# Kernel tuning notes

Measured on AMD Instinct MI355X. Metric: run time of the kernel, lower is better.

## Reference

```python
import jax, jax.numpy as jnp
import numpy as np

KNOTS = 17  # integration points on [0, 3]


def _buffers():
    t = jnp.linspace(0.0, 3.0, KNOTS, dtype=jnp.float32)
    dt = 3.0 / (KNOTS - 1)
    w = jnp.full((KNOTS,), 2.0 * dt, dtype=jnp.float32)
    w = w.at[0].set(dt).at[-1].set(dt)          # trapezoid-style end weights
    phi = jnp.exp(-jnp.square(t) / 2.0)         # ideal Gaussian ECF
    return t, phi, w * phi


def setup_inputs() -> dict:
    key = jax.random.key(0)
    k1, k2 = jax.random.split(key)
    N, D, P = 8192, 512, 1024
    z = jax.random.normal(k1, (N, D), dtype=jnp.float32)
    A = jax.random.normal(k2, (D, P), dtype=jnp.float32)  # random projections (hoisted from forward)
    return {"z": z, "A": A}


def reference(z, A):
    t, phi, weights = _buffers()
    D = z.shape[-1]
    flat = z.reshape(-1, D).astype(jnp.float32)            # [N, D]
    An = A / jnp.clip(jnp.linalg.norm(A, axis=0, keepdims=True), 1e-8)
    proj = flat @ An                                       # [N, P]
    x_t = proj[:, :, None] * t                             # [N, P, K]
    cos_mean = jnp.mean(jnp.cos(x_t), axis=0)              # [P, K]
    sin_mean = jnp.mean(jnp.sin(x_t), axis=0)              # [P, K]
    err = jnp.square(cos_mean - phi) + jnp.square(sin_mean)
    statistic = (err @ weights) * flat.shape[0]            # [P]
    return jnp.mean(statistic)
```

## Files before the change

kernel.cpp:

```cpp
#include <hip/hip_runtime.h>
#include <stdint.h>

#define N_SAMP 8192
#define D_DIM  512
#define P_DIM  1024
#define DT     0.1875f

typedef float f32x4 __attribute__((ext_vector_type(4)));
typedef float f32x2 __attribute__((ext_vector_type(2)));
typedef short bf16x8 __attribute__((ext_vector_type(8)));
typedef unsigned short u16;

__device__ __forceinline__ u16 f2bf(float x){
    unsigned int u = __float_as_uint(x);
    return (u16)((u + 0x7FFFu + ((u >> 16) & 1u)) >> 16);
}

__device__ __forceinline__ void load_lds16(const void* g, void* l){
    __builtin_amdgcn_global_load_lds(
        (const __attribute__((address_space(1))) void*)(uintptr_t)g,
        (__attribute__((address_space(3))) void*)(uint32_t)(uintptr_t)l,
        16, 0, 0);
}

__global__ __launch_bounds__(256) void k_prep(const float4* __restrict__ z4,
                                              u16* __restrict__ zb,
                                              const float* __restrict__ A,
                                              float* __restrict__ inv,
                                              u16* __restrict__ AnT,
                                              float* __restrict__ gpart,
                                              float* __restrict__ out){
    const int tid = threadIdx.x;
    const int b = blockIdx.x;
    if (b < 4096){
        int i = b * 256 + tid;
        if (i == 0) out[0] = 0.f;
        float4 v = z4[i];
        ushort4 o;
        o.x = f2bf(v.x); o.y = f2bf(v.y); o.z = f2bf(v.z); o.w = f2bf(v.w);
        ((ushort4*)zb)[i] = o;
        return;
    }
    if (b < 4128){
        __shared__ float red[8][32];
        const int p0 = (b - 4096) * 32;
        const int pl = tid & 31, dg = tid >> 5;
        float s = 0.f;
        #pragma unroll 8
        for (int i = 0; i < 64; ++i){
            float v = A[(size_t)(dg + 8 * i) * P_DIM + p0 + pl];
            s += v * v;
        }
        red[dg][pl] = s;
        __syncthreads();
        if (tid < 32){
            float t = 0.f;
            #pragma unroll
            for (int g = 0; g < 8; ++g) t += red[g][tid];
            inv[p0 + tid] = 1.0f / fmaxf(sqrtf(t), 1e-8f);
        }
        return;
    }
    if (b < 4640){
        __shared__ float tile[32][33];
        const int t = b - 4128;
        const int p0 = (t & 31) * 32, d0 = (t >> 5) * 32;
        const int tx = tid & 31, ty = tid >> 5;
        #pragma unroll
        for (int j = 0; j < 4; ++j)
            tile[ty + j * 8][tx] = A[(size_t)(d0 + ty + j * 8) * P_DIM + p0 + tx];
        __syncthreads();
        #pragma unroll
        for (int j = 0; j < 4; ++j){
            int pp = ty + j * 8;
            AnT[(size_t)(p0 + pp) * D_DIM + d0 + tx] = f2bf(tile[tx][pp]);
        }
        return;
    }
    int i = (b - 4640) * 256 + tid;
    ((float4*)gpart)[i] = (float4){0.f, 0.f, 0.f, 0.f};
}

__global__ __launch_bounds__(512) void k_gemm_ecf(const u16* __restrict__ zb,
                                                  const u16* __restrict__ AnT,
                                                  const float* __restrict__ inv,
                                                  float* __restrict__ gpart){
    __shared__ uint4 smem4[4096];
    const int tid = threadIdx.x;
    const int swz = (blockIdx.x & 7) * 64 + (blockIdx.x >> 3);
    const int bm = swz >> 3, bn = swz & 7;
    const int m0 = bm << 7, n0 = bn << 7;
    const int w = tid >> 6, lane = tid & 63;
    const int r = lane & 15, kg = lane >> 4;
    const int wm = (w >> 2) << 6;
    const int wn = (w & 3) << 5;

    const int srow = tid >> 3;
    const int gsw  = ((tid & 7) ^ (srow & 7)) << 3;
    const u16* gA = zb  + (size_t)(m0 + srow) * D_DIM + gsw;
    const u16* gB = AnT + (size_t)(n0 + srow) * D_DIM + gsw;
    char* lbase = (char*)smem4 + w * 1024;

    f32x4 acc[4][2] = {};

    #pragma unroll
    for (int h = 0; h < 2; ++h){
        load_lds16(gA + (size_t)h * 64 * D_DIM, lbase + h * 8192);
        load_lds16(gB + (size_t)h * 64 * D_DIM, lbase + 16384 + h * 8192);
    }

    for (int kt = 0; kt < 8; ++kt){
        const int cur = kt & 1;
        __syncthreads();
        if (kt < 7){
            char* la = lbase + ((kt + 1) & 1) * 32768;
            #pragma unroll
            for (int h = 0; h < 2; ++h){
                load_lds16(gA + (size_t)h * 64 * D_DIM + (kt + 1) * 64, la + h * 8192);
                load_lds16(gB + (size_t)h * 64 * D_DIM + (kt + 1) * 64, la + 16384 + h * 8192);
            }
        }
        const u16* Ab = (const u16*)smem4 + cur * 16384;
        const u16* Bb = Ab + 8192;
        #pragma unroll
        for (int ks = 0; ks < 2; ++ks){
            bf16x8 af[4], bfr[2];
            #pragma unroll
            for (int i = 0; i < 4; ++i)
                af[i] = *(const bf16x8*)&Ab[(wm + i * 16 + r) * 64 +
                                            (((ks * 4 + kg) ^ (r & 7)) << 3)];
            #pragma unroll
            for (int j = 0; j < 2; ++j)
                bfr[j] = *(const bf16x8*)&Bb[(wn + j * 16 + r) * 64 +
                                             (((ks * 4 + kg) ^ (r & 7)) << 3)];
            #pragma unroll
            for (int i = 0; i < 4; ++i)
                #pragma unroll
                for (int j = 0; j < 2; ++j)
                    acc[i][j] = __builtin_amdgcn_mfma_f32_16x16x32_bf16(
                        af[i], bfr[j], acc[i][j], 0, 0, 0);
        }
    }

    __syncthreads();
    float* epil = (float*)smem4;
    #pragma unroll
    for (int jn = 0; jn < 2; ++jn){
        const float sc = inv[n0 + wn + jn * 16 + r] * DT;
        f32x2 sum[16];
        #pragma unroll
        for (int k = 0; k < 16; ++k) sum[k] = (f32x2){0.f, 0.f};
        #pragma unroll
        for (int i = 0; i < 4; ++i){
            #pragma unroll
            for (int q = 0; q < 4; ++q){
                float x = acc[i][jn][q] * sc;
                float c1 = __cosf(x), s1 = __sinf(x);
                float tc = c1 + c1;
                f32x2 prev = {1.f, 0.f};
                f32x2 curv = {c1, s1};
                sum[0] += curv;
                #pragma unroll
                for (int k = 2; k <= 16; ++k){
                    f32x2 nxt = tc * curv - prev;
                    sum[k - 1] += nxt;
                    prev = curv; curv = nxt;
                }
            }
        }
        #pragma unroll
        for (int k = 0; k < 16; ++k){
            f32x2 o;
            o.x = __shfl_xor(sum[k].x, 16); o.y = __shfl_xor(sum[k].y, 16);
            sum[k] += o;
            o.x = __shfl_xor(sum[k].x, 32); o.y = __shfl_xor(sum[k].y, 32);
            sum[k] += o;
        }
        if (lane < 16){
            const int cl = jn * 16 + lane;
            #pragma unroll
            for (int k = 0; k < 16; ++k){
                epil[(w * 32 + k)      * 32 + cl] = sum[k].x;
                epil[(w * 32 + 16 + k) * 32 + cl] = sum[k].y;
            }
        }
    }
    __syncthreads();
    for (int f0 = 0; f0 < 4096; f0 += 512){
        int f = f0 + tid;
        int cl = f & 127, j = f >> 7;
        int whi = cl >> 5, cll = cl & 31;
        float v = epil[((whi    ) * 32 + j) * 32 + cll] +
                  epil[((whi + 4) * 32 + j) * 32 + cll];
        atomicAdd(&gpart[j * P_DIM + n0 + cl], v);
    }
}

__global__ __launch_bounds__(256) void k_reduce(const float* __restrict__ gpart,
                                                float* __restrict__ out){
    const int tid = threadIdx.x;
    const int idx = blockIdx.x * 256 + tid;
    const int j = idx >> 10;
    float s = gpart[idx];
    const int k = (j & 15) + 1;
    float tk = (float)k * DT;
    float phik = expf(-0.5f * tk * tk);
    float wk = ((k == 16) ? DT : 2.f * DT) * phik;
    float mean = s * (1.f / (float)N_SAMP);
    float diff = (j < 16) ? (mean - phik) : mean;
    float term = diff * diff * wk;
    #pragma unroll
    for (int o = 32; o > 0; o >>= 1) term += __shfl_xor(term, o);
    __shared__ float red[4];
    if ((tid & 63) == 0) red[tid >> 6] = term;
    __syncthreads();
    if (tid == 0)
        atomicAdd(out, (red[0] + red[1] + red[2] + red[3]) *
                       ((float)N_SAMP / (float)P_DIM));
}

extern "C" void kernel_launch(void* const* d_in, const int* in_sizes, int n_in,
                              void* d_out, int out_size, void* d_ws, size_t ws_size,
                              hipStream_t stream){
    const float* z = (const float*)d_in[0];
    const float* A = (const float*)d_in[1];
    char* ws = (char*)d_ws;
    float* inv   = (float*)(ws);
    float* gpart = (float*)(ws + 8192);
    u16*   AnT   = (u16*)  (ws + 139264);
    u16*   zb    = (u16*)  (ws + 1187840);
    float* out   = (float*)d_out;

    hipLaunchKernelGGL(k_prep,     dim3(4672), dim3(256), 0, stream,
                       (const float4*)z, zb, A, inv, AnT, gpart, out);
    hipLaunchKernelGGL(k_gemm_ecf, dim3(512),  dim3(512), 0, stream,
                       zb, AnT, inv, gpart);
    hipLaunchKernelGGL(k_reduce,   dim3(128),  dim3(256), 0, stream, gpart, out);
}
```

Before: 41.42 us.

## Fuse z bf16 conversion into GEMM loads and final reduction into last block

```diff
diff --git a/kernel.cpp b/kernel.cpp
--- a/kernel.cpp
+++ b/kernel.cpp
@@ -23,27 +23,22 @@
         16, 0, 0);
 }
 
-__global__ __launch_bounds__(256) void k_prep(const float4* __restrict__ z4,
-                                              u16* __restrict__ zb,
-                                              const float* __restrict__ A,
+__device__ __forceinline__ void cvt_write(char* dst, float4 a, float4 b){
+    u16 u[8] = {f2bf(a.x), f2bf(a.y), f2bf(a.z), f2bf(a.w),
+                f2bf(b.x), f2bf(b.y), f2bf(b.z), f2bf(b.w)};
+    *(uint4*)dst = *(const uint4*)u;
+}
+
+__global__ __launch_bounds__(256) void k_prep(const float* __restrict__ A,
                                               float* __restrict__ inv,
                                               u16* __restrict__ AnT,
                                               float* __restrict__ gpart,
-                                              float* __restrict__ out){
+                                              unsigned int* __restrict__ counter){
     const int tid = threadIdx.x;
     const int b = blockIdx.x;
-    if (b < 4096){
-        int i = b * 256 + tid;
-        if (i == 0) out[0] = 0.f;
-        float4 v = z4[i];
-        ushort4 o;
-        o.x = f2bf(v.x); o.y = f2bf(v.y); o.z = f2bf(v.z); o.w = f2bf(v.w);
-        ((ushort4*)zb)[i] = o;
-        return;
-    }
-    if (b < 4128){
+    if (b < 32){
         __shared__ float red[8][32];
-        const int p0 = (b - 4096) * 32;
+        const int p0 = b * 32;
         const int pl = tid & 31, dg = tid >> 5;
         float s = 0.f;
         #pragma unroll 8
@@ -61,9 +56,9 @@
         }
         return;
     }
-    if (b < 4640){
+    if (b < 544){
         __shared__ float tile[32][33];
-        const int t = b - 4128;
+        const int t = b - 32;
         const int p0 = (t & 31) * 32, d0 = (t >> 5) * 32;
         const int tx = tid & 31, ty = tid >> 5;
         #pragma unroll
@@ -77,14 +72,20 @@
         }
         return;
     }
-    int i = (b - 4640) * 256 + tid;
-    ((float4*)gpart)[i] = (float4){0.f, 0.f, 0.f, 0.f};
-}
-
-__global__ __launch_bounds__(512) void k_gemm_ecf(const u16* __restrict__ zb,
-                                                  const u16* __restrict__ AnT,
-                                                  const float* __restrict__ inv,
-                                                  float* __restrict__ gpart){
+    if (b < 576){
+        int i = (b - 544) * 256 + tid;
+        ((float4*)gpart)[i] = (float4){0.f, 0.f, 0.f, 0.f};
+        return;
+    }
+    if (tid == 0) *counter = 0u;
+}
+
+__global__ __launch_bounds__(512, 4) void k_gemm_ecf(const float* __restrict__ z,
+                                                     const u16* __restrict__ AnT,
+                                                     const float* __restrict__ inv,
+                                                     float* __restrict__ gpart,
+                                                     unsigned int* __restrict__ counter,
+                                                     float* __restrict__ out){
     __shared__ uint4 smem4[4096];
     const int tid = threadIdx.x;
     const int swz = (blockIdx.x & 7) * 64 + (blockIdx.x >> 3);
@@ -95,30 +96,42 @@
     const int wm = (w >> 2) << 6;
     const int wn = (w & 3) << 5;
 
+    const int arow = tid >> 2;
+    const int agrp = (tid & 3) << 1;
+    const int sA = arow & 7;
+    const float4* gz = (const float4*)z + (size_t)(m0 + arow) * 128 + agrp * 2;
+    const int wofs0 = arow * 128 + ((agrp     ^ sA) << 4);
+    const int wofs1 = arow * 128 + (((agrp+1) ^ sA) << 4);
+
     const int srow = tid >> 3;
     const int gsw  = ((tid & 7) ^ (srow & 7)) << 3;
-    const u16* gA = zb  + (size_t)(m0 + srow) * D_DIM + gsw;
     const u16* gB = AnT + (size_t)(n0 + srow) * D_DIM + gsw;
     char* lbase = (char*)smem4 + w * 1024;
 
     f32x4 acc[4][2] = {};
 
-    #pragma unroll
-    for (int h = 0; h < 2; ++h){
-        load_lds16(gA + (size_t)h * 64 * D_DIM, lbase + h * 8192);
-        load_lds16(gB + (size_t)h * 64 * D_DIM, lbase + 16384 + h * 8192);
+    {
+        float4 f0 = gz[0], f1 = gz[1], f2 = gz[2], f3 = gz[3];
+        char* A0 = (char*)smem4;
+        cvt_write(A0 + wofs0, f0, f1);
+        cvt_write(A0 + wofs1, f2, f3);
+        #pragma unroll
+        for (int h = 0; h < 2; ++h)
+            load_lds16(gB + (size_t)h * 64 * D_DIM, lbase + 16384 + h * 8192);
     }
 
     for (int kt = 0; kt < 8; ++kt){
         const int cur = kt & 1;
         __syncthreads();
+        float4 f0, f1, f2, f3;
         if (kt < 7){
             char* la = lbase + ((kt + 1) & 1) * 32768;
             #pragma unroll
-            for (int h = 0; h < 2; ++h){
-                load_lds16(gA + (size_t)h * 64 * D_DIM + (kt + 1) * 64, la + h * 8192);
-                load_lds16(gB + (size_t)h * 64 * D_DIM + (kt + 1) * 64, la + 16384 + h * 8192);
-            }
+            for (int h = 0; h < 2; ++h)
+                load_lds16(gB + (size_t)h * 64 * D_DIM + (kt + 1) * 64,
+                           la + 16384 + h * 8192);
+            f0 = gz[(kt + 1) * 16 + 0]; f1 = gz[(kt + 1) * 16 + 1];
+            f2 = gz[(kt + 1) * 16 + 2]; f3 = gz[(kt + 1) * 16 + 3];
         }
         const u16* Ab = (const u16*)smem4 + cur * 16384;
         const u16* Bb = Ab + 8192;
@@ -139,6 +152,11 @@
                 for (int j = 0; j < 2; ++j)
                     acc[i][j] = __builtin_amdgcn_mfma_f32_16x16x32_bf16(
                         af[i], bfr[j], acc[i][j], 0, 0, 0);
+        }
+        if (kt < 7){
+            char* An = (char*)smem4 + ((kt + 1) & 1) * 32768;
+            cvt_write(An + wofs0, f0, f1);
+            cvt_write(An + wofs1, f2, f3);
         }
     }
 
@@ -186,37 +204,45 @@
         }
     }
     __syncthreads();
-    for (int f0 = 0; f0 < 4096; f0 += 512){
-        int f = f0 + tid;
+    for (int f0i = 0; f0i < 4096; f0i += 512){
+        int f = f0i + tid;
         int cl = f & 127, j = f >> 7;
         int whi = cl >> 5, cll = cl & 31;
         float v = epil[((whi    ) * 32 + j) * 32 + cll] +
                   epil[((whi + 4) * 32 + j) * 32 + cll];
         atomicAdd(&gpart[j * P_DIM + n0 + cl], v);
     }
-}
-
-__global__ __launch_bounds__(256) void k_reduce(const float* __restrict__ gpart,
-                                                float* __restrict__ out){
-    const int tid = threadIdx.x;
-    const int idx = blockIdx.x * 256 + tid;
-    const int j = idx >> 10;
-    float s = gpart[idx];
-    const int k = (j & 15) + 1;
-    float tk = (float)k * DT;
-    float phik = expf(-0.5f * tk * tk);
-    float wk = ((k == 16) ? DT : 2.f * DT) * phik;
-    float mean = s * (1.f / (float)N_SAMP);
-    float diff = (j < 16) ? (mean - phik) : mean;
-    float term = diff * diff * wk;
-    #pragma unroll
-    for (int o = 32; o > 0; o >>= 1) term += __shfl_xor(term, o);
-    __shared__ float red[4];
-    if ((tid & 63) == 0) red[tid >> 6] = term;
+
+    __threadfence();
+    __shared__ unsigned int sticket;
+    if (tid == 0) sticket = atomicAdd(counter, 1u);
     __syncthreads();
-    if (tid == 0)
-        atomicAdd(out, (red[0] + red[1] + red[2] + red[3]) *
-                       ((float)N_SAMP / (float)P_DIM));
+    if (sticket == 511u){
+        __threadfence();
+        float part = 0.f;
+        for (int i = tid; i < 32768; i += 512){
+            const int j = i >> 10;
+            const int k = (j & 15) + 1;
+            float tk = (float)k * DT;
+            float phik = expf(-0.5f * tk * tk);
+            float wk = ((k == 16) ? DT : 2.f * DT) * phik;
+            float mean = gpart[i] * (1.f / (float)N_SAMP);
+            float diff = (j < 16) ? (mean - phik) : mean;
+            part += diff * diff * wk;
+        }
+        #pragma unroll
+        for (int o = 32; o > 0; o >>= 1) part += __shfl_xor(part, o);
+        float* red = (float*)smem4;
+        __syncthreads();
+        if (lane == 0) red[w] = part;
+        __syncthreads();
+        if (tid == 0){
+            float s = 0.f;
+            #pragma unroll
+            for (int i = 0; i < 8; ++i) s += red[i];
+            out[0] = s * ((float)N_SAMP / (float)P_DIM);
+        }
+    }
 }
 
 extern "C" void kernel_launch(void* const* d_in, const int* in_sizes, int n_in,
@@ -225,15 +251,14 @@
     const float* z = (const float*)d_in[0];
     const float* A = (const float*)d_in[1];
     char* ws = (char*)d_ws;
-    float* inv   = (float*)(ws);
-    float* gpart = (float*)(ws + 8192);
-    u16*   AnT   = (u16*)  (ws + 139264);
-    u16*   zb    = (u16*)  (ws + 1187840);
-    float* out   = (float*)d_out;
-
-    hipLaunchKernelGGL(k_prep,     dim3(4672), dim3(256), 0, stream,
-                       (const float4*)z, zb, A, inv, AnT, gpart, out);
-    hipLaunchKernelGGL(k_gemm_ecf, dim3(512),  dim3(512), 0, stream,
-                       zb, AnT, inv, gpart);
-    hipLaunchKernelGGL(k_reduce,   dim3(128),  dim3(256), 0, stream, gpart, out);
-}
+    float* inv        = (float*)(ws);
+    unsigned int* cnt = (unsigned int*)(ws + 4096);
+    float* gpart      = (float*)(ws + 8192);
+    u16*   AnT        = (u16*)  (ws + 139264);
+    float* out        = (float*)d_out;
+
+    hipLaunchKernelGGL(k_prep,     dim3(577), dim3(256), 0, stream,
+                       A, inv, AnT, gpart, cnt);
+    hipLaunchKernelGGL(k_gemm_ecf, dim3(512), dim3(512), 0, stream,
+                       z, AnT, inv, gpart, cnt, out);
+}
```

After: 107.4 us. 159% more time.
